# Kernel tuning notes

Measured on AMD Instinct MI355X. Metric: run time of the kernel, lower is better.

The kernel has to match this reference:

```python
import jax, jax.numpy as jnp
import numpy as np

EMBED = 2048
HEADS = 16
NOPE = 128      # embed // heads
VDIM = 128
ROPE = 64
Q_HEAD = NOPE + ROPE  # 192
KV_RANK = 512
BASE = 10000.0


def _rope(x, offset=0):
    # x: [b, h, n, d] with d even; rotary (lrpe_type=1) on pair-interleaved dims
    d = x.shape[-1]
    n = x.shape[-2]
    theta = BASE ** (-2.0 * jnp.arange(d // 2, dtype=jnp.float32) / d)  # [d/2]
    pos = jnp.arange(n, dtype=jnp.float32) + offset                     # [n]
    ang = pos[:, None] * theta[None, :]                                  # [n, d/2]
    cos, sin = jnp.cos(ang), jnp.sin(ang)
    x1 = x[..., 0::2]
    x2 = x[..., 1::2]
    o1 = x1 * cos - x2 * sin
    o2 = x1 * sin + x2 * cos
    return jnp.stack([o1, o2], axis=-1).reshape(x.shape)


def setup_inputs() -> dict:
    key = jax.random.key(0)
    ks = jax.random.split(key, 6)
    b, n = 2, 2048
    s = lambda fin: 1.0 / np.sqrt(fin)
    return {
        "x": jax.random.normal(ks[0], (b, n, EMBED), jnp.float32),
        "Wqa": jax.random.normal(ks[1], (EMBED, 512), jnp.float32) * s(EMBED),
        "Wqb": jax.random.normal(ks[2], (512, HEADS * Q_HEAD), jnp.float32) * s(512),
        "Wkva": jax.random.normal(ks[3], (EMBED, KV_RANK + ROPE), jnp.float32) * s(EMBED),
        "Wkvb": jax.random.normal(ks[4], (KV_RANK, HEADS * (NOPE + VDIM)), jnp.float32) * s(KV_RANK),
        "Wout": jax.random.normal(ks[5], (HEADS * VDIM, EMBED), jnp.float32) * s(HEADS * VDIM),
    }


def reference(x, Wqa, Wqb, Wkva, Wkvb, Wout):
    b, n, _ = x.shape
    # low-rank Q projection
    q = (x @ Wqa) @ Wqb                                   # [b, n, h*192]
    q = q.reshape(b, n, HEADS, Q_HEAD).transpose(0, 2, 1, 3)  # [b, h, n, 192]
    q_nope, q_pe = q[..., :NOPE], q[..., NOPE:]
    # low-rank KV compression + shared rope key
    ckv = x @ Wkva                                        # [b, n, 512+64]
    compressed, k_pe = ckv[..., :KV_RANK], ckv[..., KV_RANK:]
    k_pe = jnp.broadcast_to(k_pe[:, None], (b, HEADS, n, ROPE))
    kv = compressed @ Wkvb                                # [b, n, h*(128+128)]
    kv = kv.reshape(b, n, HEADS, NOPE + VDIM).transpose(0, 2, 1, 3)
    k_nope, v = kv[..., :NOPE], kv[..., NOPE:]
    # partial RoPE on rope slice
    q_pe = _rope(q_pe)
    k_pe = _rope(k_pe)
    qf = jnp.concatenate([q_nope, q_pe], axis=-1)         # [b, h, n, 192]
    kf = jnp.concatenate([k_nope, k_pe], axis=-1)
    # causal SDPA, scale = 1/sqrt(q_head_dim)
    scale = 1.0 / np.sqrt(Q_HEAD)
    scores = jnp.einsum("bhnd,bhmd->bhnm", qf, kf) * scale
    causal = jnp.tril(jnp.ones((n, n), dtype=bool))
    scores = jnp.where(causal, scores, jnp.finfo(scores.dtype).min)
    attn = jax.nn.softmax(scores, axis=-1)
    out = jnp.einsum("bhnm,bhmd->bhnd", attn, v)          # [b, h, n, 128]
    out = out.transpose(0, 2, 1, 3).reshape(b, n, HEADS * VDIM)
    return out @ Wout
```

## Files before the change

kernel.cpp:

```cpp
#include <hip/hip_runtime.h>
#include <math.h>

typedef __bf16 bf16;
typedef __bf16 bf16x8 __attribute__((ext_vector_type(8)));
typedef float f32x4 __attribute__((ext_vector_type(4)));

#define HEADS 16
#define QHEAD 192
#define NB 2
#define SEQ 2048
#define ROWS (NB * SEQ)
#define QSCALE2 0.10411754584f
#define CSHIFT 11.5415603272f

__global__ __launch_bounds__(256) void prep(
    const float* __restrict__ x,
    const float* __restrict__ Wqa, const float* __restrict__ Wqb,
    const float* __restrict__ Wkva, const float* __restrict__ Wkvb,
    const float* __restrict__ Wout,
    bf16* __restrict__ xb,
    bf16* __restrict__ WfT, bf16* __restrict__ WqbT,
    bf16* __restrict__ WkvbT, bf16* __restrict__ WoutT)
{
    int t = blockIdx.x;
    if (t < 8192) {
        size_t i = ((size_t)t * 256 + threadIdx.x) * 4;
        float4 v = *(const float4*)(x + i);
        xb[i]     = (bf16)v.x;
        xb[i + 1] = (bf16)v.y;
        xb[i + 2] = (bf16)v.z;
        xb[i + 3] = (bf16)v.w;
        return;
    }
    t -= 8192;
    __shared__ float tile[32][33];
    const float* in; bf16* out; int R, C;
    if (t < 1024)      {            in = Wqa;  out = WfT;                      R = 2048; C = 512;  }
    else if (t < 2176) { t -= 1024; in = Wkva; out = WfT + (size_t)512 * 2048; R = 2048; C = 576;  }
    else if (t < 3712) { t -= 2176; in = Wqb;  out = WqbT;                     R = 512;  C = 3072; }
    else if (t < 5760) { t -= 3712; in = Wkvb; out = WkvbT;                    R = 512;  C = 4096; }
    else               { t -= 5760; in = Wout; out = WoutT;                    R = 2048; C = 2048; }
    int tilesX = (C + 31) >> 5;
    int bx = (t % tilesX) * 32, by = (t / tilesX) * 32;
    int tx = threadIdx.x & 31, ty = threadIdx.x >> 5;
    for (int i = 0; i < 32; i += 8) {
        int r = by + ty + i, c = bx + tx;
        tile[ty + i][tx] = (r < R && c < C) ? in[(size_t)r * C + c] : 0.f;
    }
    __syncthreads();
    for (int i = 0; i < 32; i += 8) {
        int c = bx + ty + i, r = by + tx;
        if (c < C && r < R) out[(size_t)c * R + r] = (bf16)tile[tx][ty + i];
    }
}

#define GEMM_BODY(Aptr, LDA, Bptr, LDB, KK, BNIDX)                              \
    __shared__ bf16 As[128 * 32];                                               \
    __shared__ bf16 Bs[128 * 32];                                               \
    const int tid  = threadIdx.x;                                               \
    const int wave = tid >> 6, lane = tid & 63;                                 \
    const int quad = lane >> 4, l16 = lane & 15;                                \
    const int bm = blockIdx.x * 128, bn = (BNIDX) * 128;                        \
    const int wm = (wave >> 1) * 64, wn = (wave & 1) * 64;                      \
    const int srow = lane >> 2, scol = (lane & 3) * 8;                          \
    f32x4 acc[4][4];                                                            \
    for (int i = 0; i < 4; i++)                                                 \
        for (int j = 0; j < 4; j++)                                             \
            acc[i][j] = (f32x4){0.f, 0.f, 0.f, 0.f};                            \
    for (int k0 = 0; k0 < (KK); k0 += 32) {                                     \
        _Pragma("unroll")                                                       \
        for (int s2 = 0; s2 < 2; s2++) {                                        \
            const int seg = wave * 2 + s2;                                      \
            const bf16* ga = (Aptr) + (size_t)(bm + seg * 16 + srow) * (LDA) + k0 + scol; \
            const bf16* gb = (Bptr) + (size_t)(bn + seg * 16 + srow) * (LDB) + k0 + scol; \
            __builtin_amdgcn_global_load_lds(                                   \
                (const __attribute__((address_space(1))) void*)ga,              \
                (__attribute__((address_space(3))) void*)&As[seg * 512], 16, 0, 0); \
            __builtin_amdgcn_global_load_lds(                                   \
                (const __attribute__((address_space(1))) void*)gb,              \
                (__attribute__((address_space(3))) void*)&Bs[seg * 512], 16, 0, 0); \
        }                                                                       \
        __syncthreads();                                                        \
        bf16x8 af[4], bfv[4];                                                   \
        for (int mi = 0; mi < 4; mi++)                                          \
            af[mi] = *(const bf16x8*)&As[(wm + mi * 16 + l16) * 32 + quad * 8]; \
        for (int ni = 0; ni < 4; ni++)                                          \
            bfv[ni] = *(const bf16x8*)&Bs[(wn + ni * 16 + l16) * 32 + quad * 8];\
        for (int mi = 0; mi < 4; mi++)                                          \
            for (int ni = 0; ni < 4; ni++)                                      \
                acc[mi][ni] = __builtin_amdgcn_mfma_f32_16x16x32_bf16(          \
                    af[mi], bfv[ni], acc[mi][ni], 0, 0, 0);                     \
        __syncthreads();                                                        \
    }

template <typename OutT>
__global__ __launch_bounds__(256) void gemm_bf16(
    const bf16* __restrict__ A, int lda,
    const bf16* __restrict__ Bt, int ldb,
    OutT* __restrict__ C, int ldc,
    int N, int K)
{
    GEMM_BODY(A, lda, Bt, ldb, K, blockIdx.y)
    for (int mi = 0; mi < 4; mi++)
        for (int ni = 0; ni < 4; ni++) {
            int col = bn + wn + ni * 16 + l16;
            if (col >= N) continue;
            int row0 = bm + wm + mi * 16 + quad * 4;
            for (int r = 0; r < 4; r++)
                C[(size_t)(row0 + r) * ldc + col] = (OutT)acc[mi][ni][r];
        }
}

__global__ __launch_bounds__(256) void gemm_qkv(
    const bf16* __restrict__ tc,
    const bf16* __restrict__ WqbT, const bf16* __restrict__ WkvbT,
    bf16* __restrict__ qf, bf16* __restrict__ kf, bf16* __restrict__ kvv)
{
    const int byAll = blockIdx.y;
    const bool isQ = byAll < 24;
    const bf16* A  = isQ ? tc : tc + 512;
    const bf16* Bt = isQ ? WqbT : WkvbT;
    const int bnIdx = isQ ? byAll : byAll - 24;
    GEMM_BODY(A, 1152, Bt, 512, 512, bnIdx)
    if (isQ) {
        const bool odd = l16 & 1;
        for (int mi = 0; mi < 4; mi++)
            for (int ni = 0; ni < 4; ni++) {
                int col0 = bn + wn + ni * 16;
                int h  = col0 / 192;
                int d0 = col0 - h * 192;
                int d  = d0 + l16;
                bool roped = d0 >= 128;
                float theta = 0.f;
                if (roped) theta = powf(10000.f, -(float)((d - 128) >> 1) / 32.f);
                for (int r = 0; r < 4; r++) {
                    int row = bm + wm + mi * 16 + quad * 4 + r;
                    int b = row >> 11, n = row & 2047;
                    float v = acc[mi][ni][r], res;
                    if (roped) {
                        float p = __shfl_xor(v, 1);
                        float sn, cs;
                        sincosf((float)n * theta, &sn, &cs);
                        float x1 = odd ? p : v, x2 = odd ? v : p;
                        res = odd ? (x1 * sn + x2 * cs) : (x1 * cs - x2 * sn);
                    } else res = v;
                    qf[(((size_t)(b * HEADS + h)) * SEQ + n) * QHEAD + d] =
                        (bf16)(res * QSCALE2);
                }
            }
    } else {
        for (int mi = 0; mi < 4; mi++)
            for (int ni = 0; ni < 4; ni++) {
                int col0 = bn + wn + ni * 16;
                int h  = col0 >> 8;
                int d0 = col0 & 255;
                int d  = d0 + l16;
                for (int r = 0; r < 4; r++) {
                    int row = bm + wm + mi * 16 + quad * 4 + r;
                    int b = row >> 11, n = row & 2047;
                    bf16 v = (bf16)acc[mi][ni][r];
                    if (d0 < 128)
                        kf[(((size_t)(b * HEADS + h)) * SEQ + n) * QHEAD + d] = v;
                    else
                        kvv[(size_t)row * 2048 + h * 128 + (d - 128)] = v;
                }
            }
    }
}

__global__ __launch_bounds__(256) void rope_vt(
    const bf16* __restrict__ tc, const bf16* __restrict__ kvv,
    bf16* __restrict__ kf, bf16* __restrict__ vT)
{
    int t = blockIdx.x;
    if (t < 8192) {
        __shared__ bf16 tile[32][33];
        int bh = t >> 8, rest = t & 255;
        int dv0 = (rest >> 6) * 32, nt0 = (rest & 63) * 32;
        int b = bh >> 4, h = bh & 15;
        int tx = threadIdx.x & 31, ty = threadIdx.x >> 5;
        for (int i = 0; i < 32; i += 8) {
            int n = nt0 + ty + i;
            tile[ty + i][tx] = kvv[((size_t)(b * SEQ + n)) * 2048 + h * 128 + dv0 + tx];
        }
        __syncthreads();
        for (int i = 0; i < 32; i += 8) {
            int dv = dv0 + ty + i;
            vT[((size_t)bh * 128 + dv) * SEQ + nt0 + tx] = tile[tx][ty + i];
        }
    } else {
        int gid = (t - 8192) * 256 + threadIdx.x;
        int row = gid >> 6, j = gid & 63;
        int b = row >> 11, n = row & 2047;
        int i = j >> 1;
        float x1 = (float)tc[(size_t)row * 1152 + 1024 + 2 * i];
        float x2 = (float)tc[(size_t)row * 1152 + 1024 + 2 * i + 1];
        float theta = powf(10000.f, -(float)i / 32.f);
        float sn, cs;
        sincosf((float)n * theta, &sn, &cs);
        bf16 rv = (bf16)((j & 1) ? (x1 * sn + x2 * cs) : (x1 * cs - x2 * sn));
        for (int h = 0; h < HEADS; h++)
            kf[(((size_t)(b * HEADS + h)) * SEQ + n) * QHEAD + 128 + j] = rv;
    }
}

__global__ __launch_bounds__(256) void attn_fa(
    const bf16* __restrict__ qf, const bf16* __restrict__ kf,
    const bf16* __restrict__ vT, bf16* __restrict__ attn_out)
{
    __shared__ bf16 Ks[64][200];
    __shared__ bf16 Vt[128][72];
    __shared__ bf16 Ps[4][16][72];

    const int bid = blockIdx.x;
    const int xcd = bid & 7, j = bid >> 3;
    const int qt = 31 - (j >> 2);
    const int bh = xcd + 8 * (j & 3);
    const int b = bh >> 4, h = bh & 15;
    const int tid  = threadIdx.x;
    const int wave = tid >> 6, lane = tid & 63;
    const int quad = lane >> 4, l16 = lane & 15;

    bf16x8 aq[6];
    {
        const bf16* qbase = qf + ((size_t)bh * SEQ + qt * 64 + wave * 16 + l16) * QHEAD;
        for (int ks = 0; ks < 6; ks++)
            aq[ks] = *(const bf16x8*)(qbase + ks * 32 + quad * 8);
    }
    f32x4 o[8];
    for (int i = 0; i < 8; i++) o[i] = (f32x4){0.f, 0.f, 0.f, 0.f};
    float lp[4] = {0.f, 0.f, 0.f, 0.f};

    for (int kt = 0; kt <= qt; kt++) {
#pragma unroll
        for (int i = 0; i < 6; i++) {
            int c = tid + i * 256;
            int r = c / 24, col = (c - r * 24) * 8;
            *(uint4*)&Ks[r][col] =
                *(const uint4*)(kf + ((size_t)bh * SEQ + kt * 64 + r) * QHEAD + col);
        }
#pragma unroll
        for (int i = 0; i < 4; i++) {
            int c = tid + i * 256;
            int dv = c >> 3, g = c & 7;
            *(uint4*)&Vt[dv][g * 8] =
                *(const uint4*)(vT + ((size_t)bh * 128 + dv) * SEQ + kt * 64 + g * 8);
        }
        __syncthreads();

        f32x4 sacc[4];
        for (int nt = 0; nt < 4; nt++) sacc[nt] = (f32x4){0.f, 0.f, 0.f, 0.f};
        for (int ks = 0; ks < 6; ks++)
            for (int nt = 0; nt < 4; nt++) {
                bf16x8 bk = *(const bf16x8*)&Ks[nt * 16 + l16][ks * 32 + quad * 8];
                sacc[nt] = __builtin_amdgcn_mfma_f32_16x16x32_bf16(aq[ks], bk, sacc[nt], 0, 0, 0);
            }

        const bool diag = (kt == qt);
#pragma unroll
        for (int r = 0; r < 4; r++) {
            const int qrow = wave * 16 + quad * 4 + r;
#pragma unroll
            for (int nt = 0; nt < 4; nt++) {
                float p;
                if (diag && (nt * 16 + l16 > qrow)) p = 0.f;
                else p = __builtin_amdgcn_exp2f(sacc[nt][r] - CSHIFT);
                lp[r] += p;
                Ps[wave][quad * 4 + r][nt * 16 + l16] = (bf16)p;
            }
        }
        __builtin_amdgcn_sched_barrier(0);

        for (int ks2 = 0; ks2 < 2; ks2++) {
            bf16x8 ap = *(const bf16x8*)&Ps[wave][l16][ks2 * 32 + quad * 8];
            for (int nv = 0; nv < 8; nv++) {
                bf16x8 bv = *(const bf16x8*)&Vt[nv * 16 + l16][ks2 * 32 + quad * 8];
                o[nv] = __builtin_amdgcn_mfma_f32_16x16x32_bf16(ap, bv, o[nv], 0, 0, 0);
            }
        }
        __syncthreads();
    }

#pragma unroll
    for (int r = 0; r < 4; r++) {
        lp[r] += __shfl_xor(lp[r], 8);
        lp[r] += __shfl_xor(lp[r], 4);
        lp[r] += __shfl_xor(lp[r], 2);
        lp[r] += __shfl_xor(lp[r], 1);
    }

    for (int r = 0; r < 4; r++) {
        float inv = 1.f / lp[r];
        size_t row = (size_t)b * SEQ + qt * 64 + wave * 16 + quad * 4 + r;
        for (int nv = 0; nv < 8; nv++)
            attn_out[row * 2048 + h * 128 + nv * 16 + l16] = (bf16)(o[nv][r] * inv);
    }
}

extern "C" void kernel_launch(void* const* d_in, const int* in_sizes, int n_in,
                              void* d_out, int out_size, void* d_ws, size_t ws_size,
                              hipStream_t stream)
{
    const float* x    = (const float*)d_in[0];
    const float* Wqa  = (const float*)d_in[1];
    const float* Wqb  = (const float*)d_in[2];
    const float* Wkva = (const float*)d_in[3];
    const float* Wkvb = (const float*)d_in[4];
    const float* Wout = (const float*)d_in[5];
    float* out = (float*)d_out;

    char* ws = (char*)d_ws;
    size_t off = 0;
    auto alloc = [&](size_t elems) { char* p = ws + off; off += elems * sizeof(bf16); return (bf16*)p; };
    bf16* xb    = alloc((size_t)ROWS * 2048);
    bf16* WfT   = alloc((size_t)1152 * 2048);
    bf16* WqbT  = alloc((size_t)3072 * 512);
    bf16* WkvbT = alloc((size_t)4096 * 512);
    bf16* WoutT = alloc((size_t)2048 * 2048);
    bf16* tc    = alloc((size_t)ROWS * 1152);
    bf16* kvv   = alloc((size_t)ROWS * 2048);
    bf16* vT    = alloc((size_t)32 * 128 * SEQ);
    bf16* qf    = alloc((size_t)32 * SEQ * QHEAD);
    bf16* kf    = alloc((size_t)32 * SEQ * QHEAD);
    bf16* attn  = xb;
    if (off > ws_size) return;

    dim3 blk(256);

    prep<<<dim3(18048), blk, 0, stream>>>(x, Wqa, Wqb, Wkva, Wkvb, Wout,
                                          xb, WfT, WqbT, WkvbT, WoutT);

    gemm_bf16<bf16><<<dim3(32, 9), blk, 0, stream>>>(xb, 2048, WfT, 2048, tc, 1152, 1088, 2048);

    gemm_qkv<<<dim3(32, 56), blk, 0, stream>>>(tc, WqbT, WkvbT, qf, kf, kvv);

    rope_vt<<<dim3(9216), blk, 0, stream>>>(tc, kvv, kf, vT);

    attn_fa<<<dim3(1024), blk, 0, stream>>>(qf, kf, vT, attn);

    gemm_bf16<float><<<dim3(32, 16), blk, 0, stream>>>(attn, 2048, WoutT, 2048, out, 2048, 2048, 2048);
}
```

Baseline: 414.5 us.

## Precompute RoPE cos/sin table and register-prefetch K/V tiles in attention

Computes a RoPE cos/sin table once inside the prep kernel and has the Q-projection epilogue and the K-rope kernel read it, replacing per-element powf and sincosf. In the attention kernel, the next K/V tile is loaded into registers while the current one is being computed, so global loads overlap the MFMA work. The kernel also raises wave priority around the MFMA loops and adds a launch-bounds occupancy hint of 3. The prefetch buffers add register pressure, which the occupancy hint may constrain and cause spills, and the table adds a small global-memory read per element.

```diff
diff --git a/kernel.cpp b/kernel.cpp
--- a/kernel.cpp
+++ b/kernel.cpp
@@ -20,7 +20,8 @@
     const float* __restrict__ Wout,
     bf16* __restrict__ xb,
     bf16* __restrict__ WfT, bf16* __restrict__ WqbT,
-    bf16* __restrict__ WkvbT, bf16* __restrict__ WoutT)
+    bf16* __restrict__ WkvbT, bf16* __restrict__ WoutT,
+    float2* __restrict__ ropecs)
 {
     int t = blockIdx.x;
     if (t < 8192) {
@@ -33,6 +34,15 @@
         return;
     }
     t -= 8192;
+    if (t >= 9856) {
+        int gid = (t - 9856) * 256 + threadIdx.x;
+        int n = gid >> 5, i = gid & 31;
+        float theta = powf(10000.f, -(float)i / 32.f);
+        float sn, cs;
+        sincosf((float)n * theta, &sn, &cs);
+        ropecs[gid] = make_float2(cs, sn);
+        return;
+    }
     __shared__ float tile[32][33];
     const float* in; bf16* out; int R, C;
     if (t < 1024)      {            in = Wqa;  out = WfT;                      R = 2048; C = 512;  }
@@ -114,6 +124,7 @@
 __global__ __launch_bounds__(256) void gemm_qkv(
     const bf16* __restrict__ tc,
     const bf16* __restrict__ WqbT, const bf16* __restrict__ WkvbT,
+    const float2* __restrict__ ropecs,
     bf16* __restrict__ qf, bf16* __restrict__ kf, bf16* __restrict__ kvv)
 {
     const int byAll = blockIdx.y;
@@ -131,18 +142,16 @@
                 int d0 = col0 - h * 192;
                 int d  = d0 + l16;
                 bool roped = d0 >= 128;
-                float theta = 0.f;
-                if (roped) theta = powf(10000.f, -(float)((d - 128) >> 1) / 32.f);
+                int iidx = roped ? ((d - 128) >> 1) : 0;
                 for (int r = 0; r < 4; r++) {
                     int row = bm + wm + mi * 16 + quad * 4 + r;
                     int b = row >> 11, n = row & 2047;
                     float v = acc[mi][ni][r], res;
                     if (roped) {
                         float p = __shfl_xor(v, 1);
-                        float sn, cs;
-                        sincosf((float)n * theta, &sn, &cs);
+                        float2 cs = ropecs[n * 32 + iidx];
                         float x1 = odd ? p : v, x2 = odd ? v : p;
-                        res = odd ? (x1 * sn + x2 * cs) : (x1 * cs - x2 * sn);
+                        res = odd ? (x1 * cs.y + x2 * cs.x) : (x1 * cs.x - x2 * cs.y);
                     } else res = v;
                     qf[(((size_t)(b * HEADS + h)) * SEQ + n) * QHEAD + d] =
                         (bf16)(res * QSCALE2);
@@ -170,6 +179,7 @@
 
 __global__ __launch_bounds__(256) void rope_vt(
     const bf16* __restrict__ tc, const bf16* __restrict__ kvv,
+    const float2* __restrict__ ropecs,
     bf16* __restrict__ kf, bf16* __restrict__ vT)
 {
     int t = blockIdx.x;
@@ -195,16 +205,14 @@
         int i = j >> 1;
         float x1 = (float)tc[(size_t)row * 1152 + 1024 + 2 * i];
         float x2 = (float)tc[(size_t)row * 1152 + 1024 + 2 * i + 1];
-        float theta = powf(10000.f, -(float)i / 32.f);
-        float sn, cs;
-        sincosf((float)n * theta, &sn, &cs);
-        bf16 rv = (bf16)((j & 1) ? (x1 * sn + x2 * cs) : (x1 * cs - x2 * sn));
+        float2 cs = ropecs[n * 32 + i];
+        bf16 rv = (bf16)((j & 1) ? (x1 * cs.y + x2 * cs.x) : (x1 * cs.x - x2 * cs.y));
         for (int h = 0; h < HEADS; h++)
             kf[(((size_t)(b * HEADS + h)) * SEQ + n) * QHEAD + 128 + j] = rv;
     }
 }
 
-__global__ __launch_bounds__(256) void attn_fa(
+__global__ __launch_bounds__(256, 3) void attn_fa(
     const bf16* __restrict__ qf, const bf16* __restrict__ kf,
     const bf16* __restrict__ vT, bf16* __restrict__ attn_out)
 {
@@ -231,30 +239,49 @@
     for (int i = 0; i < 8; i++) o[i] = (f32x4){0.f, 0.f, 0.f, 0.f};
     float lp[4] = {0.f, 0.f, 0.f, 0.f};
 
+    uint4 kbuf[6], vbuf[4];
+#define PREFETCH(KT)                                                            \
+    _Pragma("unroll")                                                           \
+    for (int i = 0; i < 6; i++) {                                               \
+        int c = tid + i * 256;                                                  \
+        int r = c / 24, col = (c - r * 24) * 8;                                 \
+        kbuf[i] = *(const uint4*)(kf + ((size_t)bh * SEQ + (KT) * 64 + r) * QHEAD + col); \
+    }                                                                           \
+    _Pragma("unroll")                                                           \
+    for (int i = 0; i < 4; i++) {                                               \
+        int c = tid + i * 256;                                                  \
+        int dv = c >> 3, g = c & 7;                                             \
+        vbuf[i] = *(const uint4*)(vT + ((size_t)bh * 128 + dv) * SEQ + (KT) * 64 + g * 8); \
+    }
+
+    PREFETCH(0)
+
     for (int kt = 0; kt <= qt; kt++) {
+        __syncthreads();
 #pragma unroll
         for (int i = 0; i < 6; i++) {
             int c = tid + i * 256;
             int r = c / 24, col = (c - r * 24) * 8;
-            *(uint4*)&Ks[r][col] =
-                *(const uint4*)(kf + ((size_t)bh * SEQ + kt * 64 + r) * QHEAD + col);
+            *(uint4*)&Ks[r][col] = kbuf[i];
         }
 #pragma unroll
         for (int i = 0; i < 4; i++) {
             int c = tid + i * 256;
             int dv = c >> 3, g = c & 7;
-            *(uint4*)&Vt[dv][g * 8] =
-                *(const uint4*)(vT + ((size_t)bh * 128 + dv) * SEQ + kt * 64 + g * 8);
+            *(uint4*)&Vt[dv][g * 8] = vbuf[i];
         }
         __syncthreads();
+        if (kt < qt) { PREFETCH(kt + 1) }
 
         f32x4 sacc[4];
         for (int nt = 0; nt < 4; nt++) sacc[nt] = (f32x4){0.f, 0.f, 0.f, 0.f};
+        __builtin_amdgcn_s_setprio(1);
         for (int ks = 0; ks < 6; ks++)
             for (int nt = 0; nt < 4; nt++) {
                 bf16x8 bk = *(const bf16x8*)&Ks[nt * 16 + l16][ks * 32 + quad * 8];
                 sacc[nt] = __builtin_amdgcn_mfma_f32_16x16x32_bf16(aq[ks], bk, sacc[nt], 0, 0, 0);
             }
+        __builtin_amdgcn_s_setprio(0);
 
         const bool diag = (kt == qt);
 #pragma unroll
@@ -271,6 +298,7 @@
         }
         __builtin_amdgcn_sched_barrier(0);
 
+        __builtin_amdgcn_s_setprio(1);
         for (int ks2 = 0; ks2 < 2; ks2++) {
             bf16x8 ap = *(const bf16x8*)&Ps[wave][l16][ks2 * 32 + quad * 8];
             for (int nv = 0; nv < 8; nv++) {
@@ -278,8 +306,9 @@
                 o[nv] = __builtin_amdgcn_mfma_f32_16x16x32_bf16(ap, bv, o[nv], 0, 0, 0);
             }
         }
-        __syncthreads();
-    }
+        __builtin_amdgcn_s_setprio(0);
+    }
+#undef PREFETCH
 
 #pragma unroll
     for (int r = 0; r < 4; r++) {
@@ -323,18 +352,20 @@
     bf16* qf    = alloc((size_t)32 * SEQ * QHEAD);
     bf16* kf    = alloc((size_t)32 * SEQ * QHEAD);
     bf16* attn  = xb;
+    float2* ropecs = (float2*)(ws + off);
+    off += (size_t)SEQ * 32 * sizeof(float2);
     if (off > ws_size) return;
 
     dim3 blk(256);
 
-    prep<<<dim3(18048), blk, 0, stream>>>(x, Wqa, Wqb, Wkva, Wkvb, Wout,
-                                          xb, WfT, WqbT, WkvbT, WoutT);
+    prep<<<dim3(18304), blk, 0, stream>>>(x, Wqa, Wqb, Wkva, Wkvb, Wout,
+                                          xb, WfT, WqbT, WkvbT, WoutT, ropecs);
 
     gemm_bf16<bf16><<<dim3(32, 9), blk, 0, stream>>>(xb, 2048, WfT, 2048, tc, 1152, 1088, 2048);
 
-    gemm_qkv<<<dim3(32, 56), blk, 0, stream>>>(tc, WqbT, WkvbT, qf, kf, kvv);
-
-    rope_vt<<<dim3(9216), blk, 0, stream>>>(tc, kvv, kf, vT);
+    gemm_qkv<<<dim3(32, 56), blk, 0, stream>>>(tc, WqbT, WkvbT, ropecs, qf, kf, kvv);
+
+    rope_vt<<<dim3(9216), blk, 0, stream>>>(tc, kvv, ropecs, kf, vT);
 
     attn_fa<<<dim3(1024), blk, 0, stream>>>(qf, kf, vT, attn);
 
```

New measurement: 794.4 us. +91.7%, slower.
